# Kernel optimization log

Hardware: AMD Instinct MI355X
Metric: run time of the kernel (lower is better)

## Reference

```python
import jax, jax.numpy as jnp
import numpy as np
import math

B, S, L, H, NH, FF, V = 32, 512, 12, 768, 12, 3072, 30522
DH = H // NH


def setup_inputs() -> dict:
    key = jax.random.key(0)
    ks = jax.random.split(key, 16)
    w = lambda k, shape: (jax.random.normal(k, shape, jnp.float32) * 0.02)
    return {
        "input_ids": jax.random.randint(ks[0], (B, S), 0, V, dtype=jnp.int32),
        "attention_mask": jax.random.uniform(ks[1], (B, S), jnp.float32),
        "word_emb": w(ks[2], (V, H)),
        "pos_emb": w(ks[3], (S, H)),
        "type_emb": w(ks[4], (H,)),
        "ln_emb_s": jnp.ones((H,), jnp.float32),
        "ln_emb_b": jnp.zeros((H,), jnp.float32),
        "Wq": w(ks[5], (L, H, H)), "bq": jnp.zeros((L, H), jnp.float32),
        "Wk": w(ks[6], (L, H, H)), "bk": jnp.zeros((L, H), jnp.float32),
        "Wv": w(ks[7], (L, H, H)), "bv": jnp.zeros((L, H), jnp.float32),
        "Wo": w(ks[8], (L, H, H)), "bo": jnp.zeros((L, H), jnp.float32),
        "ln1_s": jnp.ones((L, H), jnp.float32), "ln1_b": jnp.zeros((L, H), jnp.float32),
        "Wi": w(ks[9], (L, H, FF)), "bi": jnp.zeros((L, FF), jnp.float32),
        "Wf": w(ks[10], (L, FF, H)), "bf": jnp.zeros((L, H), jnp.float32),
        "ln2_s": jnp.ones((L, H), jnp.float32), "ln2_b": jnp.zeros((L, H), jnp.float32),
    }


def _ln(x, s, b):
    # BERT LayerNorm, eps=1e-12
    m = jnp.mean(x, -1, keepdims=True)
    v = jnp.mean((x - m) ** 2, -1, keepdims=True)
    return (x - m) * jax.lax.rsqrt(v + 1e-12) * s + b


def reference(input_ids, attention_mask, word_emb, pos_emb, type_emb,
              ln_emb_s, ln_emb_b, Wq, bq, Wk, bk, Wv, bv, Wo, bo,
              ln1_s, ln1_b, Wi, bi, Wf, bf, ln2_s, ln2_b):
    b, s = input_ids.shape
    scale = 1.0 / math.sqrt(DH)
    # Embeddings: word + position + (single) token-type, then LayerNorm
    h = word_emb[input_ids] + pos_emb[None, :s] + type_emb
    h = _ln(h, ln_emb_s, ln_emb_b)
    key_mask = attention_mask[:, None, None, :]  # [B,1,1,S], float

    def layer(h, p):
        wq, bq_, wk, bk_, wv, bv_, wo, bo_, l1s, l1b, wi, bi_, wf, bf_, l2s, l2b = p
        q = (jnp.einsum('bsd,de->bse', h, wq) + bq_).reshape(b, s, NH, DH)
        k = (jnp.einsum('bsd,de->bse', h, wk) + bk_).reshape(b, s, NH, DH)
        v = (jnp.einsum('bsd,de->bse', h, wv) + bv_).reshape(b, s, NH, DH)
        scores = jnp.einsum('bqhd,bkhd->bhqk', q, k) * scale
        probs = jax.nn.softmax(scores, axis=-1)
        # post-softmax masking + renormalization (the non-standard part)
        probs = probs * key_mask
        probs = probs / jnp.clip(jnp.sum(probs, -1, keepdims=True), 1e-9, None)
        ctx = jnp.einsum('bhqk,bkhd->bqhd', probs, v).reshape(b, s, H)
        attn_out = _ln(jnp.einsum('bsd,de->bse', ctx, wo) + bo_ + h, l1s, l1b)
        inter = jax.nn.gelu(jnp.einsum('bsd,df->bsf', attn_out, wi) + bi_, approximate=False)
        out = _ln(jnp.einsum('bsf,fd->bsd', inter, wf) + bf_ + attn_out, l2s, l2b)
        return out, None

    h, _ = jax.lax.scan(layer, h, (Wq, bq, Wk, bk, Wv, bv, Wo, bo,
                                   ln1_s, ln1_b, Wi, bi, Wf, bf, ln2_s, ln2_b))
    # masked mean pooling + L2 normalize (normalize=True)
    m = attention_mask[..., None]
    sent = jnp.sum(h * m, axis=1) / jnp.clip(jnp.sum(m, axis=1), 1e-6, None)
    sent = sent / jnp.clip(jnp.linalg.norm(sent, axis=-1, keepdims=True), 1e-12, None)
    return sent
```

## Files before the change

### kernel.cpp

```cpp
#include <hip/hip_runtime.h>
#include <hip/hip_bf16.h>
#include <math.h>

typedef __bf16 bf16;
typedef __bf16 bf16x8 __attribute__((ext_vector_type(8)));
typedef float  f32x4  __attribute__((ext_vector_type(4)));

#define B_  32
#define S_  512
#define H_  768
#define NH_ 12
#define DH_ 64
#define FF_ 3072
#define L_  12
#define M_  (B_*S_)
#define QKV_ 2304

#define VST 516
#define PST 68

__device__ __forceinline__ void gload16(const bf16* g, bf16* l) {
  __builtin_amdgcn_global_load_lds(
      (const __attribute__((address_space(1))) void*)g,
      (__attribute__((address_space(3))) void*)l, 16, 0, 0);
}

__device__ __forceinline__ float fast_gelu(float x) {
  float z = x * 0.70710678118f;
  float s = fabsf(z);
  float t = __builtin_amdgcn_rcpf(1.0f + 0.3275911f * s);
  float p = t*(0.254829592f + t*(-0.284496736f + t*(1.421413741f +
            t*(-1.453152027f + t*1.061405429f))));
  float e = p * __expf(-s*s);
  float erfv = copysignf(1.0f - e, z);
  return 0.5f * x * (1.0f + erfv);
}

__global__ __launch_bounds__(512, 4) void gemm128(
    const bf16* __restrict__ A, const bf16* __restrict__ Bt,
    const float* __restrict__ bias, void* __restrict__ outp,
    int N, int K, int tiles_n, int epi)
{
  __shared__ bf16 As[128*64];
  __shared__ bf16 Bs[128*64];
  const int tid  = threadIdx.x;
  const int lane = tid & 63, wid = tid >> 6;
  const int wr = wid >> 2, wc = wid & 3;
  const int lrow = lane & 15, kgrp = lane >> 4;

  const int nwg = gridDim.x, orig = blockIdx.x;
  const int qc = nwg >> 3, rc = nwg & 7;
  const int xcd = orig & 7, lin = orig >> 3;
  const int wg = (xcd < rc ? xcd*(qc+1) : rc*(qc+1) + (xcd-rc)*qc) + lin;
  const int tm = wg / tiles_n, tn = wg % tiles_n;
  const size_t m0 = (size_t)tm * 128, n0 = (size_t)tn * 128;
  const int KT = K >> 6;

  const bf16* Ab = A  + m0 * K;
  const bf16* Bb = Bt + n0 * K;

  auto stage = [&](const bf16* gbase, bf16* ldsbase, int kt) {
#pragma unroll
    for (int j = 0; j < 2; ++j) {
      int lin2  = j*512 + tid;
      int prow  = lin2 >> 3;
      int pslot = lin2 & 7;
      int lslot = pslot ^ (prow & 7);
      const bf16* src = gbase + (size_t)prow * K + (size_t)kt*64 + lslot*8;
      bf16* dst = ldsbase + (size_t)(j*512 + (wid<<6))*8;
      gload16(src, dst);
    }
  };

  f32x4 acc[4][2] = {};

  for (int t = 0; t < KT; ++t) {
    __syncthreads();
    stage(Ab, As, t);
    stage(Bb, Bs, t);
    __syncthreads();
#pragma unroll
    for (int kk = 0; kk < 2; ++kk) {
      bf16x8 a[4], b[2];
#pragma unroll
      for (int m = 0; m < 4; ++m) {
        int row  = wr*64 + m*16 + lrow;
        int slot = (kk*4 + kgrp) ^ (lrow & 7);
        a[m] = *(const bf16x8*)&As[row*64 + slot*8];
      }
#pragma unroll
      for (int n = 0; n < 2; ++n) {
        int row  = wc*32 + n*16 + lrow;
        int slot = (kk*4 + kgrp) ^ (lrow & 7);
        b[n] = *(const bf16x8*)&Bs[row*64 + slot*8];
      }
#pragma unroll
      for (int m = 0; m < 4; ++m)
#pragma unroll
        for (int n = 0; n < 2; ++n)
          acc[m][n] = __builtin_amdgcn_mfma_f32_16x16x32_bf16(a[m], b[n], acc[m][n], 0, 0, 0);
    }
  }

#pragma unroll
  for (int m = 0; m < 4; ++m)
#pragma unroll
    for (int n = 0; n < 2; ++n) {
      int col = (int)n0 + wc*32 + n*16 + lrow;
      float bv = bias[col];
#pragma unroll
      for (int r = 0; r < 4; ++r) {
        int row = (int)m0 + wr*64 + m*16 + kgrp*4 + r;
        float x = acc[m][n][r] + bv;
        size_t idx = (size_t)row * N + col;
        if (epi == 1)      ((float*)outp)[idx] = x;
        else if (epi == 0) ((bf16*)outp)[idx]  = (bf16)x;
        else               ((bf16*)outp)[idx]  = (bf16)fast_gelu(x);
      }
    }
}

__global__ __launch_bounds__(256) void weight_prep(
    const float* __restrict__ Wq, const float* __restrict__ Wk,
    const float* __restrict__ Wv, const float* __restrict__ Wo,
    const float* __restrict__ Wi, const float* __restrict__ Wf,
    const float* __restrict__ bq, const float* __restrict__ bk,
    const float* __restrict__ bv,
    bf16* __restrict__ wqkv, bf16* __restrict__ wot,
    bf16* __restrict__ wit,  bf16* __restrict__ wft,
    float* __restrict__ qkbias)
{
  int bid = blockIdx.x;
  if (bid >= 1728) {
    int i = (bid - 1728)*256 + threadIdx.x;
    if (i < QKV_)
      qkbias[i] = (i < 768) ? bq[i] : (i < 1536 ? bk[i-768] : bv[i-1536]);
    return;
  }
  const float* W; bf16* Wt; int K, N, t;
  if (bid < 576) {
    K = 768; N = 768;
    if      (bid < 144) { W = Wq; Wt = wqkv;             t = bid; }
    else if (bid < 288) { W = Wk; Wt = wqkv + 768*768;   t = bid - 144; }
    else if (bid < 432) { W = Wv; Wt = wqkv + 2*768*768; t = bid - 288; }
    else                { W = Wo; Wt = wot;              t = bid - 432; }
  } else if (bid < 1152) { W = Wi; Wt = wit; K = 768;  N = 3072; t = bid - 576; }
  else                   { W = Wf; Wt = wft; K = 3072; N = 768;  t = bid - 1152; }
  const int kt = K >> 6;
  const int k0 = (t % kt)*64, n0 = (t / kt)*64;

  __shared__ bf16 T[64][65];
  int tx = threadIdx.x & 63, ty = threadIdx.x >> 6;
#pragma unroll
  for (int j = 0; j < 16; ++j) {
    int kk = j*4 + ty;
    T[kk][tx] = (bf16)W[(size_t)(k0+kk)*N + n0 + tx];
  }
  __syncthreads();
#pragma unroll
  for (int j = 0; j < 16; ++j) {
    int nn = j*4 + ty;
    Wt[(size_t)(n0+nn)*K + k0 + tx] = T[tx][nn];
  }
}

__device__ __forceinline__ void block_sum2(float& a, float& b, float* red) {
  int lane = threadIdx.x & 63, wid = threadIdx.x >> 6;
  for (int o = 32; o > 0; o >>= 1) { a += __shfl_xor(a, o); b += __shfl_xor(b, o); }
  if (lane == 0) { red[wid*2] = a; red[wid*2+1] = b; }
  __syncthreads();
  a = red[0] + red[2] + red[4] + red[6];
  b = red[1] + red[3] + red[5] + red[7];
  __syncthreads();
}

__global__ __launch_bounds__(256) void embed_ln(
    const int* __restrict__ ids, const float* __restrict__ we,
    const float* __restrict__ pe, const float* __restrict__ te,
    const float* __restrict__ gs, const float* __restrict__ gb,
    float* __restrict__ h32, bf16* __restrict__ hb)
{
  __shared__ float red[8];
  int row = blockIdx.x;
  int s = row & (S_-1);
  int id = ids[row];
  int t = threadIdx.x;
  float x[3], sum = 0.f, sq = 0.f;
#pragma unroll
  for (int j = 0; j < 3; ++j) {
    int c = t + j*256;
    float v = we[(size_t)id*H_ + c] + pe[(size_t)s*H_ + c] + te[c];
    x[j] = v; sum += v; sq += v*v;
  }
  block_sum2(sum, sq, red);
  float mean = sum * (1.f/H_);
  float var  = sq  * (1.f/H_) - mean*mean;
  float rstd = rsqrtf(fmaxf(var, 0.f) + 1e-12f);
#pragma unroll
  for (int j = 0; j < 3; ++j) {
    int c = t + j*256;
    float y = (x[j]-mean)*rstd*gs[c] + gb[c];
    h32[(size_t)row*H_ + c] = y;
    hb [(size_t)row*H_ + c] = (bf16)y;
  }
}

__global__ __launch_bounds__(256) void ln_res(
    const bf16* __restrict__ t16, const float* __restrict__ res,
    const float* __restrict__ gs, const float* __restrict__ gb,
    float* __restrict__ o32, bf16* __restrict__ ob)
{
  __shared__ float red[8];
  int row = blockIdx.x, t = threadIdx.x;
  float x[3], sum = 0.f, sq = 0.f;
#pragma unroll
  for (int j = 0; j < 3; ++j) {
    int c = t + j*256;
    float v = (float)t16[(size_t)row*H_ + c] + res[(size_t)row*H_ + c];
    x[j] = v; sum += v; sq += v*v;
  }
  block_sum2(sum, sq, red);
  float mean = sum * (1.f/H_);
  float var  = sq  * (1.f/H_) - mean*mean;
  float rstd = rsqrtf(fmaxf(var, 0.f) + 1e-12f);
#pragma unroll
  for (int j = 0; j < 3; ++j) {
    int c = t + j*256;
    float y = (x[j]-mean)*rstd*gs[c] + gb[c];
    o32[(size_t)row*H_ + c] = y;
    ob [(size_t)row*H_ + c] = (bf16)y;
  }
}

__global__ __launch_bounds__(512, 2) void attn_kernel(
    const bf16* __restrict__ qkv, const float* __restrict__ mask,
    bf16* __restrict__ ctx)
{
  __shared__ bf16 Kl[S_*64];
  __shared__ bf16 Vt[DH_*VST];
  __shared__ float mk[S_];
  __shared__ bf16 Pl[8][16*PST];
  int tid = threadIdx.x, lane = tid & 63, wid = tid >> 6;
  int lrow = lane & 15, kgrp = lane >> 4;
  int cur_head = -1;

  bf16x8 onesv;
#pragma unroll
  for (int i = 0; i < 8; ++i) onesv[i] = (bf16)1.0f;

  for (int u = 0; u < 6; ++u) {
    int unit = blockIdx.x*6 + u;
    int hh = unit >> 2, pass = unit & 3;
    int b = hh / NH_, h = hh % NH_;
    const bf16* Qb = qkv + (size_t)(b*S_)*QKV_ + h*DH_;

    if (hh != cur_head) {
      __syncthreads();
      const bf16* Kb = qkv + (size_t)(b*S_)*QKV_ + H_   + h*DH_;
      const bf16* Vb = qkv + (size_t)(b*S_)*QKV_ + 2*H_ + h*DH_;
#pragma unroll
      for (int it = 0; it < 8; ++it) {
        int lin   = it*512 + tid;
        int prow  = lin >> 3;
        int pslot = lin & 7;
        int lslot = pslot ^ (prow & 7);
        gload16(&Kb[(size_t)prow*QKV_ + lslot*8],
                &Kl[(size_t)(it*512 + (wid<<6))*8]);
      }
      for (int it = 0; it < 8; ++it) {
        int slot = it*512 + tid;
        int s = slot >> 3, c8 = (slot & 7)*8;
        bf16x8 v = *(const bf16x8*)&Vb[(size_t)s*QKV_ + c8];
#pragma unroll
        for (int i = 0; i < 8; ++i) Vt[(c8+i)*VST + s] = v[i];
      }
      mk[tid] = mask[b*S_ + tid];
      cur_head = hh;
      __syncthreads();
    }

    int q0 = pass*128 + wid*16;
    bf16x8 qa[2];
#pragma unroll
    for (int kc = 0; kc < 2; ++kc) {
      qa[kc] = *(const bf16x8*)&Qb[(size_t)(q0 + lrow)*QKV_ + kc*32 + kgrp*8];
#pragma unroll
      for (int i = 0; i < 8; ++i)
        qa[kc][i] = (bf16)((float)qa[kc][i] * 0.125f);
    }
    f32x4 O[4] = {};
    f32x4 O5 = {};
    float mrun[4];
#pragma unroll
    for (int r = 0; r < 4; ++r) mrun[r] = -1e30f;

    for (int c0 = 0; c0 < S_; c0 += 64) {
      f32x4 Sf[4] = {};
      __builtin_amdgcn_s_setprio(1);
#pragma unroll
      for (int kc = 0; kc < 2; ++kc)
#pragma unroll
        for (int sn = 0; sn < 4; ++sn) {
          int row  = c0 + sn*16 + lrow;
          int slot = (kc*4 + kgrp) ^ (lrow & 7);
          bf16x8 kbv = *(const bf16x8*)&Kl[(size_t)row*64 + slot*8];
          Sf[sn] = __builtin_amdgcn_mfma_f32_16x16x32_bf16(qa[kc], kbv, Sf[sn], 0, 0, 0);
        }
      __builtin_amdgcn_s_setprio(0);

      float lm[4];
#pragma unroll
      for (int r = 0; r < 4; ++r)
        lm[r] = fmaxf(fmaxf(Sf[0][r], Sf[1][r]), fmaxf(Sf[2][r], Sf[3][r]));
      bool small = (lm[0] <= mrun[0]+8.f) && (lm[1] <= mrun[1]+8.f) &&
                   (lm[2] <= mrun[2]+8.f) && (lm[3] <= mrun[3]+8.f);
      bool skip = __all(small);
      float newm[4];
      if (skip) {
#pragma unroll
        for (int r = 0; r < 4; ++r) newm[r] = mrun[r];
      } else {
        float cmax[4];
#pragma unroll
        for (int r = 0; r < 4; ++r) cmax[r] = lm[r];
        for (int o = 1; o < 16; o <<= 1)
#pragma unroll
          for (int r = 0; r < 4; ++r) cmax[r] = fmaxf(cmax[r], __shfl_xor(cmax[r], o));
#pragma unroll
        for (int r = 0; r < 4; ++r) {
          newm[r] = fmaxf(mrun[r], cmax[r]);
          float fr = __expf(mrun[r] - newm[r]);
#pragma unroll
          for (int on = 0; on < 4; ++on) O[on][r] *= fr;
          O5[r] *= fr;
          mrun[r] = newm[r];
        }
      }
#pragma unroll
      for (int sn = 0; sn < 4; ++sn) {
        float mkv = mk[c0 + sn*16 + lrow];
#pragma unroll
        for (int r = 0; r < 4; ++r) {
          float e = __expf(Sf[sn][r] - newm[r]) * mkv;
          Pl[wid][(kgrp*4 + r)*PST + sn*16 + lrow] = (bf16)e;
        }
      }
      asm volatile("s_waitcnt lgkmcnt(0)" ::: "memory");
      __builtin_amdgcn_sched_barrier(0);
      __builtin_amdgcn_s_setprio(1);
#pragma unroll
      for (int kc = 0; kc < 2; ++kc) {
        bf16x8 pa = *(const bf16x8*)&Pl[wid][lrow*PST + kc*32 + kgrp*8];
#pragma unroll
        for (int on = 0; on < 4; ++on) {
          bf16x8 vv = *(const bf16x8*)&Vt[(on*16 + lrow)*VST + c0 + kc*32 + kgrp*8];
          O[on] = __builtin_amdgcn_mfma_f32_16x16x32_bf16(pa, vv, O[on], 0, 0, 0);
        }
        O5 = __builtin_amdgcn_mfma_f32_16x16x32_bf16(pa, onesv, O5, 0, 0, 0);
      }
      __builtin_amdgcn_s_setprio(0);
    }
#pragma unroll
    for (int on = 0; on < 4; ++on)
#pragma unroll
      for (int r = 0; r < 4; ++r) {
        float val = O[on][r] / fmaxf(O5[r], 1e-9f);
        int q = q0 + kgrp*4 + r;
        ctx[(size_t)(b*S_ + q)*H_ + h*DH_ + on*16 + lrow] = (bf16)val;
      }
  }
}

__global__ __launch_bounds__(256) void pool_partial(
    const float* __restrict__ h32, const float* __restrict__ mask,
    float* __restrict__ part)
{
  int b = blockIdx.x >> 3, ch = blockIdx.x & 7;
  int t = threadIdx.x;
  float a0 = 0.f, a1 = 0.f, a2 = 0.f;
  for (int s = ch*64; s < ch*64 + 64; ++s) {
    float m = mask[b*S_ + s];
    const float* hp = &h32[((size_t)b*S_ + s)*H_];
    a0 += hp[t]*m; a1 += hp[t+256]*m; a2 += hp[t+512]*m;
  }
  float* pp = &part[(size_t)(b*8 + ch)*H_];
  pp[t] = a0; pp[t+256] = a1; pp[t+512] = a2;
}

__global__ __launch_bounds__(256) void pool_final(
    const float* __restrict__ part, const float* __restrict__ mask,
    float* __restrict__ out)
{
  __shared__ float red[8];
  int b = blockIdx.x, t = threadIdx.x;
  float s0 = 0.f, s1 = 0.f, s2 = 0.f;
#pragma unroll
  for (int ch = 0; ch < 8; ++ch) {
    const float* pp = &part[(size_t)(b*8 + ch)*H_];
    s0 += pp[t]; s1 += pp[t+256]; s2 += pp[t+512];
  }
  float msum = mask[b*S_ + t] + mask[b*S_ + 256 + t];
  float dummy = 0.f;
  block_sum2(msum, dummy, red);
  float inv = 1.f / fmaxf(msum, 1e-6f);
  s0 *= inv; s1 *= inv; s2 *= inv;
  float nrm = s0*s0 + s1*s1 + s2*s2;
  dummy = 0.f;
  block_sum2(nrm, dummy, red);
  float rn = 1.f / fmaxf(sqrtf(nrm), 1e-12f);
  out[b*H_ + t]       = s0*rn;
  out[b*H_ + t + 256] = s1*rn;
  out[b*H_ + t + 512] = s2*rn;
}

extern "C" void kernel_launch(void* const* d_in, const int* in_sizes, int n_in,
                              void* d_out, int out_size, void* d_ws, size_t ws_size,
                              hipStream_t stream)
{
  const int*   ids  = (const int*)  d_in[0];
  const float* mask = (const float*)d_in[1];
  const float* we   = (const float*)d_in[2];
  const float* pe   = (const float*)d_in[3];
  const float* te   = (const float*)d_in[4];
  const float* les  = (const float*)d_in[5];
  const float* leb  = (const float*)d_in[6];
  const float* Wq   = (const float*)d_in[7];
  const float* bq   = (const float*)d_in[8];
  const float* Wk   = (const float*)d_in[9];
  const float* bk   = (const float*)d_in[10];
  const float* Wv   = (const float*)d_in[11];
  const float* bv   = (const float*)d_in[12];
  const float* Wo   = (const float*)d_in[13];
  const float* bo   = (const float*)d_in[14];
  const float* l1s  = (const float*)d_in[15];
  const float* l1b  = (const float*)d_in[16];
  const float* Wi   = (const float*)d_in[17];
  const float* bi   = (const float*)d_in[18];
  const float* Wf   = (const float*)d_in[19];
  const float* bfp  = (const float*)d_in[20];
  const float* l2s  = (const float*)d_in[21];
  const float* l2b  = (const float*)d_in[22];

  char* p = (char*)d_ws;
  auto alloc = [&](size_t bytes) { char* q = p; p += (bytes + 255) & ~(size_t)255; return q; };
  bf16*  wqkv = (bf16*) alloc((size_t)QKV_*H_*2);
  bf16*  wot  = (bf16*) alloc((size_t)H_*H_*2);
  bf16*  wit  = (bf16*) alloc((size_t)H_*FF_*2);
  bf16*  wft  = (bf16*) alloc((size_t)H_*FF_*2);
  float* qkbias=(float*)alloc((size_t)QKV_*4);
  bf16*  hb   = (bf16*) alloc((size_t)M_*H_*2);
  float* h32  = (float*)alloc((size_t)M_*H_*4);
  float* a32  = (float*)alloc((size_t)M_*H_*4);
  bf16*  tmpb = (bf16*) alloc((size_t)M_*H_*2);
  bf16*  qkvb = (bf16*) alloc((size_t)M_*QKV_*2);
  bf16*  cxb  = (bf16*) alloc((size_t)M_*H_*2);
  bf16*  inb  = (bf16*) alloc((size_t)M_*FF_*2);
  float* part = (float*)alloc((size_t)B_*8*H_*4);

  embed_ln<<<M_, 256, 0, stream>>>(ids, we, pe, te, les, leb, h32, hb);

  for (int l = 0; l < L_; ++l) {
    size_t wsq = (size_t)l*H_*H_;
    weight_prep<<<1737, 256, 0, stream>>>(
        Wq + wsq, Wk + wsq, Wv + wsq, Wo + wsq,
        Wi + (size_t)l*H_*FF_, Wf + (size_t)l*FF_*H_,
        bq + l*H_, bk + l*H_, bv + l*H_,
        wqkv, wot, wit, wft, qkbias);

    gemm128<<<128*(QKV_/128), 512, 0, stream>>>(hb,  wqkv, qkbias,      qkvb, QKV_, H_,  QKV_/128, 0);
    attn_kernel<<<256, 512, 0, stream>>>(qkvb, mask, cxb);
    gemm128<<<128*(H_/128),  512, 0, stream>>>(cxb, wot, bo  + l*H_,  tmpb, H_,  H_,  H_/128,  0);
    ln_res<<<M_, 256, 0, stream>>>(tmpb, h32, l1s + l*H_, l1b + l*H_, a32, hb);
    gemm128<<<128*(FF_/128), 512, 0, stream>>>(hb,  wit, bi  + l*FF_, inb,  FF_, H_,  FF_/128, 2);
    gemm128<<<128*(H_/128),  512, 0, stream>>>(inb, wft, bfp + l*H_,  tmpb, H_,  FF_, H_/128,  0);
    ln_res<<<M_, 256, 0, stream>>>(tmpb, a32, l2s + l*H_, l2b + l*H_, h32, hb);
  }

  pool_partial<<<B_*8, 256, 0, stream>>>(h32, mask, part);
  pool_final<<<B_, 256, 0, stream>>>(part, mask, (float*)d_out);
}
```

Before: 4.964 ms.

## Add 256x128-tile GEMM for QKV and FFN-up, loosen attention loop scheduling

Adds a gemm256 kernel. Each block computes a 256x128 output tile with 8 waves, and each wave holds a 4x4 grid of MFMA accumulators. The QKV projection and FFN-up projection now use it, which raises arithmetic intensity per LDS load and halves the number of blocks. The attention kernel's key-chunk loop is unrolled by 2, and the explicit lgkmcnt wait and sched_barrier between writing P and the PV MFMAs are removed, giving the compiler more scheduling freedom. The larger tile needs more registers and LDS (launch bounds cut to 2 blocks/CU) and still uses single-buffered loads. Dropping the explicit wait leaves the ordering of P writes and reads to the compiler.

Result: no change. 4.977 ms (+0.2%).

```diff
diff --git a/kernel.cpp b/kernel.cpp
--- a/kernel.cpp
+++ b/kernel.cpp
@@ -34,6 +34,93 @@
   float e = p * __expf(-s*s);
   float erfv = copysignf(1.0f - e, z);
   return 0.5f * x * (1.0f + erfv);
+}
+
+__global__ __launch_bounds__(512, 2) void gemm256(
+    const bf16* __restrict__ A, const bf16* __restrict__ Bt,
+    const float* __restrict__ bias, void* __restrict__ outp,
+    int N, int K, int tiles_n, int epi)
+{
+  __shared__ bf16 As[256*64];
+  __shared__ bf16 Bs[128*64];
+  const int tid  = threadIdx.x;
+  const int lane = tid & 63, wid = tid >> 6;
+  const int wr = wid >> 1, wc = wid & 1;
+  const int lrow = lane & 15, kgrp = lane >> 4;
+
+  const int nwg = gridDim.x, orig = blockIdx.x;
+  const int qc = nwg >> 3, rc = nwg & 7;
+  const int xcd = orig & 7, lin = orig >> 3;
+  const int wg = (xcd < rc ? xcd*(qc+1) : rc*(qc+1) + (xcd-rc)*qc) + lin;
+  const int tm = wg / tiles_n, tn = wg % tiles_n;
+  const size_t m0 = (size_t)tm * 256, n0 = (size_t)tn * 128;
+  const int KT = K >> 6;
+
+  const bf16* Ab = A  + m0 * K;
+  const bf16* Bb = Bt + n0 * K;
+
+  f32x4 acc[4][4] = {};
+
+  for (int t = 0; t < KT; ++t) {
+    __syncthreads();
+#pragma unroll
+    for (int j = 0; j < 4; ++j) {
+      int lin2  = j*512 + tid;
+      int prow  = lin2 >> 3;
+      int pslot = lin2 & 7;
+      int lslot = pslot ^ (prow & 7);
+      gload16(Ab + (size_t)prow * K + (size_t)t*64 + lslot*8,
+              As + (size_t)(j*512 + (wid<<6))*8);
+    }
+#pragma unroll
+    for (int j = 0; j < 2; ++j) {
+      int lin2  = j*512 + tid;
+      int prow  = lin2 >> 3;
+      int pslot = lin2 & 7;
+      int lslot = pslot ^ (prow & 7);
+      gload16(Bb + (size_t)prow * K + (size_t)t*64 + lslot*8,
+              Bs + (size_t)(j*512 + (wid<<6))*8);
+    }
+    __syncthreads();
+#pragma unroll
+    for (int kk = 0; kk < 2; ++kk) {
+      bf16x8 a[4], b[4];
+#pragma unroll
+      for (int m = 0; m < 4; ++m) {
+        int row  = wr*64 + m*16 + lrow;
+        int slot = (kk*4 + kgrp) ^ (lrow & 7);
+        a[m] = *(const bf16x8*)&As[row*64 + slot*8];
+      }
+#pragma unroll
+      for (int n = 0; n < 4; ++n) {
+        int row  = wc*64 + n*16 + lrow;
+        int slot = (kk*4 + kgrp) ^ (lrow & 7);
+        b[n] = *(const bf16x8*)&Bs[row*64 + slot*8];
+      }
+#pragma unroll
+      for (int m = 0; m < 4; ++m)
+#pragma unroll
+        for (int n = 0; n < 4; ++n)
+          acc[m][n] = __builtin_amdgcn_mfma_f32_16x16x32_bf16(a[m], b[n], acc[m][n], 0, 0, 0);
+    }
+  }
+
+#pragma unroll
+  for (int m = 0; m < 4; ++m)
+#pragma unroll
+    for (int n = 0; n < 4; ++n) {
+      int col = (int)n0 + wc*64 + n*16 + lrow;
+      float bv = bias[col];
+#pragma unroll
+      for (int r = 0; r < 4; ++r) {
+        int row = (int)m0 + wr*64 + m*16 + kgrp*4 + r;
+        float x = acc[m][n][r] + bv;
+        size_t idx = (size_t)row * N + col;
+        if (epi == 1)      ((float*)outp)[idx] = x;
+        else if (epi == 0) ((bf16*)outp)[idx]  = (bf16)x;
+        else               ((bf16*)outp)[idx]  = (bf16)fast_gelu(x);
+      }
+    }
 }
 
 __global__ __launch_bounds__(512, 4) void gemm128(
@@ -294,6 +381,7 @@
 #pragma unroll
     for (int r = 0; r < 4; ++r) mrun[r] = -1e30f;
 
+#pragma unroll 2
     for (int c0 = 0; c0 < S_; c0 += 64) {
       f32x4 Sf[4] = {};
       __builtin_amdgcn_s_setprio(1);
@@ -345,8 +433,6 @@
           Pl[wid][(kgrp*4 + r)*PST + sn*16 + lrow] = (bf16)e;
         }
       }
-      asm volatile("s_waitcnt lgkmcnt(0)" ::: "memory");
-      __builtin_amdgcn_sched_barrier(0);
       __builtin_amdgcn_s_setprio(1);
 #pragma unroll
       for (int kc = 0; kc < 2; ++kc) {
@@ -467,11 +553,11 @@
         bq + l*H_, bk + l*H_, bv + l*H_,
         wqkv, wot, wit, wft, qkbias);
 
-    gemm128<<<128*(QKV_/128), 512, 0, stream>>>(hb,  wqkv, qkbias,      qkvb, QKV_, H_,  QKV_/128, 0);
+    gemm256<<<64*(QKV_/128), 512, 0, stream>>>(hb,  wqkv, qkbias,      qkvb, QKV_, H_,  QKV_/128, 0);
     attn_kernel<<<256, 512, 0, stream>>>(qkvb, mask, cxb);
     gemm128<<<128*(H_/128),  512, 0, stream>>>(cxb, wot, bo  + l*H_,  tmpb, H_,  H_,  H_/128,  0);
     ln_res<<<M_, 256, 0, stream>>>(tmpb, h32, l1s + l*H_, l1b + l*H_, a32, hb);
-    gemm128<<<128*(FF_/128), 512, 0, stream>>>(hb,  wit, bi  + l*FF_, inb,  FF_, H_,  FF_/128, 2);
+    gemm256<<<64*(FF_/128),  512, 0, stream>>>(hb,  wit, bi  + l*FF_, inb,  FF_, H_,  FF_/128, 2);
     gemm128<<<128*(H_/128),  512, 0, stream>>>(inb, wft, bfp + l*H_,  tmpb, H_,  FF_, H_/128,  0);
     ln_res<<<M_, 256, 0, stream>>>(tmpb, a32, l2s + l*H_, l2b + l*H_, h32, hb);
   }
```
